# Kernel tuning notes

Measured on AMD Instinct MI355X. Metric: run time of the kernel, lower is better.

## Reference

```python
import jax, jax.numpy as jnp
import numpy as np

INPUT_SIZE = 512
HIDDEN_SIZE = 1024
OUTPUT_SIZE = 2
SEQ_LENGTH = 64
BATCH = 2048


def setup_inputs() -> dict:
    key = jax.random.key(0)
    ks = jax.random.split(key, 9)
    cin = INPUT_SIZE + HIDDEN_SIZE
    s = 1.0 / np.sqrt(cin)
    x = jax.random.normal(ks[0], (BATCH, SEQ_LENGTH, INPUT_SIZE), dtype=jnp.float32)
    Wf = jax.random.uniform(ks[1], (HIDDEN_SIZE, cin), jnp.float32, -s, s)
    bf = jax.random.uniform(ks[2], (HIDDEN_SIZE,), jnp.float32, -s, s)
    Wg = jax.random.uniform(ks[3], (HIDDEN_SIZE, cin), jnp.float32, -s, s)
    bg = jax.random.uniform(ks[4], (HIDDEN_SIZE,), jnp.float32, -s, s)
    Wh = jax.random.uniform(ks[5], (HIDDEN_SIZE, cin), jnp.float32, -s, s)
    bh = jax.random.uniform(ks[6], (HIDDEN_SIZE,), jnp.float32, -s, s)
    sf = 1.0 / np.sqrt(HIDDEN_SIZE)
    Wfc = jax.random.uniform(ks[7], (OUTPUT_SIZE, HIDDEN_SIZE), jnp.float32, -sf, sf)
    bfc = jax.random.uniform(ks[8], (OUTPUT_SIZE,), jnp.float32, -sf, sf)
    return {"x": x, "Wf": Wf, "bf": bf, "Wg": Wg, "bg": bg,
            "Wh": Wh, "bh": bh, "Wfc": Wfc, "bfc": bfc}


def _lnn_forward(x, Wf, bf, Wg, bg, Wh, bh, Wfc, bfc):
    B = x.shape[0]
    h0 = jnp.zeros((B, Wf.shape[0]), dtype=x.dtype)
    xs = jnp.swapaxes(x, 0, 1)  # [T, B, D]

    def step(h, xt):
        combined = jnp.concatenate([xt, h], axis=-1)  # [B, D+H]
        f_out = combined @ Wf.T + bf
        g_out = combined @ Wg.T + bg
        h_out = combined @ Wh.T + bh
        gate = jax.nn.sigmoid(-f_out)
        new_h = gate * g_out + (1.0 - gate) * h_out
        return new_h, None

    h_final, _ = jax.lax.scan(step, h0, xs)
    return h_final @ Wfc.T + bfc  # [B, output_size]


def reference(x, Wf, bf, Wg, bg, Wh, bh, Wfc, bfc):
    return _lnn_forward(x, Wf, bf, Wg, bg, Wh, bh, Wfc, bfc)
```

## Files before the change

kernel.cpp:

```cpp
#include <hip/hip_runtime.h>

#define BATCH 2048
#define TSEQ  64
#define DIN   512
#define HID   1024
#define CIN   1536

#define BM 128
#define BN 64
#define BK 64
#define KITERS (CIN / BK)

#define CHUNK   1088
#define A_CHUNKS 16
#define B_CHUNKS 8
#define A_BYTES (A_CHUNKS * CHUNK)
#define B_MAT   (B_CHUNKS * CHUNK)
#define BUF_BYTES (A_BYTES + 3 * B_MAT)

typedef __attribute__((ext_vector_type(8))) short bf16x8;
typedef __attribute__((ext_vector_type(4))) float f32x4;
typedef __attribute__((ext_vector_type(4))) float fvec4;
typedef __attribute__((ext_vector_type(4))) unsigned int uvec4;

__device__ __forceinline__ unsigned short f2bf(float f) {
    unsigned int u = __float_as_uint(f);
    u += 0x7fffu + ((u >> 16) & 1u);
    return (unsigned short)(u >> 16);
}
__device__ __forceinline__ float bf2f(unsigned short u) {
    return __uint_as_float(((unsigned int)u) << 16);
}

__device__ __forceinline__ void gload_lds16(const void* g, void* lds) {
    __builtin_amdgcn_global_load_lds(
        (const __attribute__((address_space(1))) void*)(uintptr_t)g,
        (__attribute__((address_space(3))) void*)(unsigned)(uintptr_t)lds,
        16, 0, 0);
}

__global__ __launch_bounds__(256) void convert_w(const float* __restrict__ Wf,
                                                 const float* __restrict__ Wg,
                                                 const float* __restrict__ Wh,
                                                 unsigned short* __restrict__ Wb) {
    int mat = blockIdx.y;
    const float* src = (mat == 0) ? Wf : ((mat == 1) ? Wg : Wh);
    size_t base = (size_t)mat * (size_t)(HID * CIN);
    size_t idx = ((size_t)blockIdx.x * 256 + threadIdx.x) * 8;
    const fvec4* s = (const fvec4*)(src + idx);
    fvec4 a = s[0], b = s[1];
    uvec4 o;
    o.x = (unsigned)f2bf(a.x) | ((unsigned)f2bf(a.y) << 16);
    o.y = (unsigned)f2bf(a.z) | ((unsigned)f2bf(a.w) << 16);
    o.z = (unsigned)f2bf(b.x) | ((unsigned)f2bf(b.y) << 16);
    o.w = (unsigned)f2bf(b.z) | ((unsigned)f2bf(b.w) << 16);
    *(uvec4*)(Wb + base + idx) = o;
}

__global__ __launch_bounds__(256) void convert_x(const float* __restrict__ x,
                                                 unsigned short* __restrict__ xb) {
    size_t e = ((size_t)blockIdx.x * 256 + threadIdx.x) * 8;
    int t   = (int)(e / ((size_t)BATCH * DIN));
    int rem = (int)(e % ((size_t)BATCH * DIN));
    int b = rem / DIN;
    int d = rem % DIN;
    const float* src = x + ((size_t)b * TSEQ + t) * DIN + d;
    fvec4 a = *(const fvec4*)src;
    fvec4 c = *(const fvec4*)(src + 4);
    uvec4 o;
    o.x = (unsigned)f2bf(a.x) | ((unsigned)f2bf(a.y) << 16);
    o.y = (unsigned)f2bf(a.z) | ((unsigned)f2bf(a.w) << 16);
    o.z = (unsigned)f2bf(c.x) | ((unsigned)f2bf(c.y) << 16);
    o.w = (unsigned)f2bf(c.z) | ((unsigned)f2bf(c.w) << 16);
    *(uvec4*)(xb + e) = o;
}

__global__ __launch_bounds__(256, 1) void step_kernel(
    const unsigned short* __restrict__ xb,
    const unsigned short* __restrict__ Wb,
    const float* __restrict__ bfv,
    const float* __restrict__ bgv,
    const float* __restrict__ bhv,
    const unsigned short* __restrict__ hin,
    unsigned short* __restrict__ hout,
    int t)
{
    __shared__ __align__(16) char lds[2][BUF_BYTES];

    const int tid  = threadIdx.x;
    const int bid  = blockIdx.x;
    const int n_tile = ((bid & 7) << 1) | ((bid >> 3) & 1);
    const int m_tile = bid >> 4;
    const int m0 = m_tile * BM;
    const int n0 = n_tile * BN;

    const int lane = tid & 63;
    const int wave = tid >> 6;
    const int wm = wave >> 1;
    const int wn = wave & 1;

    const int drow = lane >> 3;
    const int dcol = (lane & 7) * 8;

    f32x4 acc[3][4][2] = {};

    float biasF[2], biasG[2], biasH[2];
#pragma unroll
    for (int nt = 0; nt < 2; ++nt) {
        int cg = n0 + wn * 32 + nt * 16 + (lane & 15);
        biasF[nt] = bfv[cg];
        biasG[nt] = bgv[cg];
        biasH[nt] = bhv[cg];
    }

    const unsigned short* xsrc = xb + (size_t)t * BATCH * DIN;

    int aoff[4], boff[2];
#pragma unroll
    for (int mt = 0; mt < 4; ++mt) {
        int r = wm * 64 + mt * 16 + (lane & 15);
        aoff[mt] = (r >> 3) * CHUNK + (r & 7) * 128;
    }
#pragma unroll
    for (int nt = 0; nt < 2; ++nt) {
        int n = wn * 32 + nt * 16 + (lane & 15);
        boff[nt] = (n >> 3) * CHUNK + (n & 7) * 128;
    }
    const int kboff = (lane >> 4) * 16;

    auto stage = [&](int ki, int bb) {
        char* base = lds[bb];
        const int k0 = ki * BK;
        const unsigned short* asrc;
        int astride;
        if (k0 < DIN) { asrc = xsrc + k0;        astride = DIN; }
        else          { asrc = hin + (k0 - DIN); astride = HID; }
#pragma unroll
        for (int c = 0; c < 4; ++c) {
            int chunk = wave * 4 + c;
            gload_lds16(asrc + (size_t)(m0 + chunk * 8 + drow) * astride + dcol,
                        base + chunk * CHUNK);
        }
#pragma unroll
        for (int mat = 0; mat < 3; ++mat) {
            const unsigned short* bsrc = Wb + (size_t)mat * (HID * CIN) + k0;
#pragma unroll
            for (int c = 0; c < 2; ++c) {
                int chunk = wave * 2 + c;
                gload_lds16(bsrc + (size_t)(n0 + chunk * 8 + drow) * CIN + dcol,
                            base + A_BYTES + mat * B_MAT + chunk * CHUNK);
            }
        }
    };

    auto compute = [&](int bb) {
        const char* base = lds[bb];
#pragma unroll
        for (int ks = 0; ks < 2; ++ks) {
            const int kb = ks * 64 + kboff;
            bf16x8 af[4];
#pragma unroll
            for (int mt = 0; mt < 4; ++mt)
                af[mt] = *(const bf16x8*)(base + aoff[mt] + kb);
#pragma unroll
            for (int mat = 0; mat < 3; ++mat) {
                const char* bmat = base + A_BYTES + mat * B_MAT;
                bf16x8 b0 = *(const bf16x8*)(bmat + boff[0] + kb);
                bf16x8 b1 = *(const bf16x8*)(bmat + boff[1] + kb);
#pragma unroll
                for (int mt = 0; mt < 4; ++mt) {
                    acc[mat][mt][0] = __builtin_amdgcn_mfma_f32_16x16x32_bf16(af[mt], b0, acc[mat][mt][0], 0, 0, 0);
                    acc[mat][mt][1] = __builtin_amdgcn_mfma_f32_16x16x32_bf16(af[mt], b1, acc[mat][mt][1], 0, 0, 0);
                }
            }
        }
    };

    stage(0, 0);
    for (int ki = 0; ki < KITERS; ++ki) {
        const int bb = ki & 1;
        __syncthreads();
        if (ki < KITERS - 1) stage(ki + 1, bb ^ 1);
        compute(bb);
    }

#pragma unroll
    for (int mt = 0; mt < 4; ++mt) {
        int rbase = m0 + wm * 64 + mt * 16 + (lane >> 4) * 4;
#pragma unroll
        for (int nt = 0; nt < 2; ++nt) {
            int cg = n0 + wn * 32 + nt * 16 + (lane & 15);
#pragma unroll
            for (int r = 0; r < 4; ++r) {
                float f  = acc[0][mt][nt][r] + biasF[nt];
                float g  = acc[1][mt][nt][r] + biasG[nt];
                float hh = acc[2][mt][nt][r] + biasH[nt];
                float gate = 1.0f / (1.0f + __expf(f));
                float nh = hh + gate * (g - hh);
                __builtin_nontemporal_store(f2bf(nh),
                    hout + (size_t)(rbase + r) * HID + cg);
            }
        }
    }
}

__global__ __launch_bounds__(256) void fc_kernel(const unsigned short* __restrict__ h,
                                                 const float* __restrict__ Wfc,
                                                 const float* __restrict__ bfc,
                                                 float* __restrict__ out) {
    int row = blockIdx.x;
    int tid = threadIdx.x;
    const unsigned short* hr = h + (size_t)row * HID;
    ushort4 hv = *(const ushort4*)(hr + tid * 4);
    float h0 = bf2f(hv.x), h1 = bf2f(hv.y), h2 = bf2f(hv.z), h3 = bf2f(hv.w);
    float4 w0 = *(const float4*)(Wfc + tid * 4);
    float4 w1 = *(const float4*)(Wfc + HID + tid * 4);
    float a0 = h0 * w0.x + h1 * w0.y + h2 * w0.z + h3 * w0.w;
    float a1 = h0 * w1.x + h1 * w1.y + h2 * w1.z + h3 * w1.w;
#pragma unroll
    for (int off = 32; off > 0; off >>= 1) {
        a0 += __shfl_down(a0, off);
        a1 += __shfl_down(a1, off);
    }
    __shared__ float red[2][4];
    if ((tid & 63) == 0) { red[0][tid >> 6] = a0; red[1][tid >> 6] = a1; }
    __syncthreads();
    if (tid == 0) out[(size_t)row * 2 + 0] = red[0][0] + red[0][1] + red[0][2] + red[0][3] + bfc[0];
    if (tid == 1) out[(size_t)row * 2 + 1] = red[1][0] + red[1][1] + red[1][2] + red[1][3] + bfc[1];
}

extern "C" void kernel_launch(void* const* d_in, const int* in_sizes, int n_in,
                              void* d_out, int out_size, void* d_ws, size_t ws_size,
                              hipStream_t stream) {
    const float* x   = (const float*)d_in[0];
    const float* Wf  = (const float*)d_in[1];
    const float* bfv = (const float*)d_in[2];
    const float* Wg  = (const float*)d_in[3];
    const float* bgv = (const float*)d_in[4];
    const float* Wh  = (const float*)d_in[5];
    const float* bhv = (const float*)d_in[6];
    const float* Wfc = (const float*)d_in[7];
    const float* bfc = (const float*)d_in[8];
    float* out = (float*)d_out;

    char* ws = (char*)d_ws;
    unsigned short* Wb = (unsigned short*)ws;
    size_t wb_bytes = (size_t)3 * HID * CIN * 2;
    size_t h_bytes  = (size_t)BATCH * HID * 2;
    unsigned short* h0 = (unsigned short*)(ws + wb_bytes);
    unsigned short* h1 = (unsigned short*)(ws + wb_bytes + h_bytes);
    unsigned short* xbuf = (unsigned short*)(ws + wb_bytes + 2 * h_bytes);

    convert_w<<<dim3(768, 3), 256, 0, stream>>>(Wf, Wg, Wh, Wb);
    convert_x<<<32768, 256, 0, stream>>>(x, xbuf);
    (void)hipMemsetAsync(h0, 0, h_bytes, stream);

    unsigned short* bufs[2] = {h0, h1};
    for (int t = 0; t < TSEQ; ++t) {
        step_kernel<<<256, 256, 0, stream>>>(xbuf, Wb, bfv, bgv, bhv,
                                             bufs[t & 1], bufs[(t + 1) & 1], t);
    }
    fc_kernel<<<BATCH, 256, 0, stream>>>(h0, Wfc, bfc, out);
}
```

Measured before the change: 2.242 ms.

## Halve step-kernel N tile to launch 512 blocks with two blocks per CU

Shrinks the per-block output tile from 128x64 to 128x32 columns, which doubles the grid of each recurrent step from 256 to 512 blocks. Launch bounds now allow two blocks per CU, and the smaller accumulator array and LDS buffer make that fit. The B-tile staging is redistributed across waves and the block-to-tile mapping is updated to match. The aim is to fill all CUs on the MI355X and overlap memory latency across blocks. The cost is that each A tile is now loaded from global memory twice as often, and each MFMA gets less operand reuse per loaded fragment.

```diff
diff --git a/kernel.cpp b/kernel.cpp
--- a/kernel.cpp
+++ b/kernel.cpp
@@ -7,13 +7,13 @@
 #define CIN   1536
 
 #define BM 128
-#define BN 64
+#define BN 32
 #define BK 64
 #define KITERS (CIN / BK)
 
 #define CHUNK   1088
 #define A_CHUNKS 16
-#define B_CHUNKS 8
+#define B_CHUNKS 4
 #define A_BYTES (A_CHUNKS * CHUNK)
 #define B_MAT   (B_CHUNKS * CHUNK)
 #define BUF_BYTES (A_BYTES + 3 * B_MAT)
@@ -75,7 +75,7 @@
     *(uvec4*)(xb + e) = o;
 }
 
-__global__ __launch_bounds__(256, 1) void step_kernel(
+__global__ __launch_bounds__(256, 2) void step_kernel(
     const unsigned short* __restrict__ xb,
     const unsigned short* __restrict__ Wb,
     const float* __restrict__ bfv,
@@ -89,8 +89,8 @@
 
     const int tid  = threadIdx.x;
     const int bid  = blockIdx.x;
-    const int n_tile = ((bid & 7) << 1) | ((bid >> 3) & 1);
-    const int m_tile = bid >> 4;
+    const int n_tile = ((bid & 7) << 2) | ((bid >> 3) & 3);
+    const int m_tile = bid >> 5;
     const int m0 = m_tile * BM;
     const int n0 = n_tile * BN;
 
@@ -102,30 +102,23 @@
     const int drow = lane >> 3;
     const int dcol = (lane & 7) * 8;
 
-    f32x4 acc[3][4][2] = {};
-
-    float biasF[2], biasG[2], biasH[2];
-#pragma unroll
-    for (int nt = 0; nt < 2; ++nt) {
-        int cg = n0 + wn * 32 + nt * 16 + (lane & 15);
-        biasF[nt] = bfv[cg];
-        biasG[nt] = bgv[cg];
-        biasH[nt] = bhv[cg];
-    }
+    f32x4 acc[3][4] = {};
+
+    const int cg = n0 + wn * 16 + (lane & 15);
+    const float biasF = bfv[cg];
+    const float biasG = bgv[cg];
+    const float biasH = bhv[cg];
 
     const unsigned short* xsrc = xb + (size_t)t * BATCH * DIN;
 
-    int aoff[4], boff[2];
+    int aoff[4];
 #pragma unroll
     for (int mt = 0; mt < 4; ++mt) {
         int r = wm * 64 + mt * 16 + (lane & 15);
         aoff[mt] = (r >> 3) * CHUNK + (r & 7) * 128;
     }
-#pragma unroll
-    for (int nt = 0; nt < 2; ++nt) {
-        int n = wn * 32 + nt * 16 + (lane & 15);
-        boff[nt] = (n >> 3) * CHUNK + (n & 7) * 128;
-    }
+    const int nloc = wn * 16 + (lane & 15);
+    const int boff = (nloc >> 3) * CHUNK + (nloc & 7) * 128;
     const int kboff = (lane >> 4) * 16;
 
     auto stage = [&](int ki, int bb) {
@@ -142,14 +135,12 @@
                         base + chunk * CHUNK);
         }
 #pragma unroll
-        for (int mat = 0; mat < 3; ++mat) {
-            const unsigned short* bsrc = Wb + (size_t)mat * (HID * CIN) + k0;
-#pragma unroll
-            for (int c = 0; c < 2; ++c) {
-                int chunk = wave * 2 + c;
-                gload_lds16(bsrc + (size_t)(n0 + chunk * 8 + drow) * CIN + dcol,
-                            base + A_BYTES + mat * B_MAT + chunk * CHUNK);
-            }
+        for (int j = 0; j < 3; ++j) {
+            int u = wave * 3 + j;
+            int mat = u >> 2, chunk = u & 3;
+            gload_lds16(Wb + (size_t)mat * (HID * CIN) + (size_t)(n0 + chunk * 8 + drow) * CIN
+                           + k0 + dcol,
+                        base + A_BYTES + mat * B_MAT + chunk * CHUNK);
         }
     };
 
@@ -164,14 +155,11 @@
                 af[mt] = *(const bf16x8*)(base + aoff[mt] + kb);
 #pragma unroll
             for (int mat = 0; mat < 3; ++mat) {
-                const char* bmat = base + A_BYTES + mat * B_MAT;
-                bf16x8 b0 = *(const bf16x8*)(bmat + boff[0] + kb);
-                bf16x8 b1 = *(const bf16x8*)(bmat + boff[1] + kb);
-#pragma unroll
-                for (int mt = 0; mt < 4; ++mt) {
-                    acc[mat][mt][0] = __builtin_amdgcn_mfma_f32_16x16x32_bf16(af[mt], b0, acc[mat][mt][0], 0, 0, 0);
-                    acc[mat][mt][1] = __builtin_amdgcn_mfma_f32_16x16x32_bf16(af[mt], b1, acc[mat][mt][1], 0, 0, 0);
-                }
+                bf16x8 bq = *(const bf16x8*)(base + A_BYTES + mat * B_MAT + boff + kb);
+#pragma unroll
+                for (int mt = 0; mt < 4; ++mt)
+                    acc[mat][mt] = __builtin_amdgcn_mfma_f32_16x16x32_bf16(
+                        af[mt], bq, acc[mat][mt], 0, 0, 0);
             }
         }
     };
@@ -188,18 +176,14 @@
     for (int mt = 0; mt < 4; ++mt) {
         int rbase = m0 + wm * 64 + mt * 16 + (lane >> 4) * 4;
 #pragma unroll
-        for (int nt = 0; nt < 2; ++nt) {
-            int cg = n0 + wn * 32 + nt * 16 + (lane & 15);
-#pragma unroll
-            for (int r = 0; r < 4; ++r) {
-                float f  = acc[0][mt][nt][r] + biasF[nt];
-                float g  = acc[1][mt][nt][r] + biasG[nt];
-                float hh = acc[2][mt][nt][r] + biasH[nt];
-                float gate = 1.0f / (1.0f + __expf(f));
-                float nh = hh + gate * (g - hh);
-                __builtin_nontemporal_store(f2bf(nh),
-                    hout + (size_t)(rbase + r) * HID + cg);
-            }
+        for (int r = 0; r < 4; ++r) {
+            float f  = acc[0][mt][r] + biasF;
+            float g  = acc[1][mt][r] + biasG;
+            float hh = acc[2][mt][r] + biasH;
+            float gate = 1.0f / (1.0f + __expf(f));
+            float nh = hh + gate * (g - hh);
+            __builtin_nontemporal_store(f2bf(nh),
+                hout + (size_t)(rbase + r) * HID + cg);
         }
     }
 }
@@ -257,7 +241,7 @@
 
     unsigned short* bufs[2] = {h0, h1};
     for (int t = 0; t < TSEQ; ++t) {
-        step_kernel<<<256, 256, 0, stream>>>(xbuf, Wb, bfv, bgv, bhv,
+        step_kernel<<<512, 256, 0, stream>>>(xbuf, Wb, bfv, bgv, bhv,
                                              bufs[t & 1], bufs[(t + 1) & 1], t);
     }
     fc_kernel<<<BATCH, 256, 0, stream>>>(h0, Wfc, bfc, out);
```

Result: faster. 1.982 ms (-11.6%).
